# Kernel optimization log

Measured on AMD Instinct MI355X. Metric: run time of the kernel, lower is better.

## Reference

```python
import jax, jax.numpy as jnp
import numpy as np

N = 8192
F_IN = 256
F_OUT = 64
ALPHA = 0.2  # LeakyReLU negative slope
MASK_VAL = -9e15


def setup_inputs() -> dict:
    key = jax.random.key(0)
    k1, k2, k3, k4 = jax.random.split(key, 4)
    h = jax.random.normal(k1, (N, F_IN), dtype=jnp.float32)
    adj = jax.random.randint(k2, (N, N), 0, 2, dtype=jnp.int32)  # 0/1 dense adjacency
    # Parameters (original creates them inside forward with xavier init; here fixed inputs)
    W = jax.random.normal(k3, (F_IN, F_OUT), dtype=jnp.float32) * (1.414 * np.sqrt(2.0 / (F_IN + F_OUT)))
    a = jax.random.normal(k4, (2 * F_OUT, 1), dtype=jnp.float32) * (1.414 * np.sqrt(2.0 / (2 * F_OUT + 1)))
    return {"h": h, "adj": adj, "W": W, "a": a}


def reference(h, adj, W, a):
    # Wh: [N, F_OUT]
    Wh = h @ W
    # e_ij = LeakyReLU(a^T [Wh_i ; Wh_j]) computed via broadcast instead of the
    f_src = Wh @ a[:F_OUT, 0]   # [N] contribution of row node i
    f_dst = Wh @ a[F_OUT:, 0]   # [N] contribution of col node j
    e = jax.nn.leaky_relu(f_src[:, None] + f_dst[None, :], negative_slope=ALPHA)  # [N, N]
    # adj-masked row softmax
    scores = jnp.where(adj > 0, e, MASK_VAL)
    attention = jax.nn.softmax(scores, axis=1)
    # dropout omitted (deterministic eval reference)
    h_prime = attention @ Wh  # [N, F_OUT]
    return jax.nn.elu(h_prime)  # concat=True branch
```

## Files before the change

kernel.cpp:

```cpp
#include <hip/hip_runtime.h>
#include <hip/hip_bf16.h>

#define NN 8192
#define FIN 256
#define FOUT 64

typedef __attribute__((ext_vector_type(8))) short short8;
typedef __attribute__((ext_vector_type(4))) float f32x4;
typedef __attribute__((ext_vector_type(4))) int   iv4;

__device__ __forceinline__ unsigned short f2bf(float x){
  unsigned u = __float_as_uint(x);
  u += 0x7FFFu + ((u >> 16) & 1u);
  return (unsigned short)(u >> 16);
}

__global__ __launch_bounds__(256) void k_prep(const float* __restrict__ h,
    const float* __restrict__ W, const float* __restrict__ a,
    unsigned short* __restrict__ WhT, float* __restrict__ fs,
    float* __restrict__ fd, unsigned* __restrict__ gmax_u){
  __shared__ float Ws[128*64];
  __shared__ float hs[8][128];
  const int t = threadIdx.x, l = t & 63, wv = t >> 6;
  const int rb = blockIdx.x * 8;
  float acc0 = 0.f, acc1 = 0.f;
  for (int half = 0; half < 2; ++half){
    if (half) __syncthreads();
    for (int i = t; i < 2048; i += 256)
      ((float4*)Ws)[i] = ((const float4*)W)[half*2048 + i];
    {
      int rr = t >> 5, cc = t & 31;
      ((float4*)&hs[rr][0])[cc] =
          *(const float4*)(h + (size_t)(rb+rr)*FIN + half*128 + cc*4);
    }
    __syncthreads();
    #pragma unroll 8
    for (int k = 0; k < 128; ++k){
      float wval = Ws[k*64 + l];
      acc0 = fmaf(hs[wv*2+0][k], wval, acc0);
      acc1 = fmaf(hs[wv*2+1][k], wval, acc1);
    }
  }
  const int r0 = rb + wv*2, r1 = r0 + 1;
  float a1 = a[l], a2 = a[64 + l];
  float p0 = acc0*a1, q0 = acc0*a2, p1 = acc1*a1, q1 = acc1*a2;
  #pragma unroll
  for (int m = 1; m < 64; m <<= 1){
    p0 += __shfl_xor(p0, m); q0 += __shfl_xor(q0, m);
    p1 += __shfl_xor(p1, m); q1 += __shfl_xor(q1, m);
  }
  if (l == 0){
    fs[r0] = p0; fs[r1] = p1; fd[r0] = q0; fd[r1] = q1;
    atomicMax(gmax_u, __float_as_uint(q0 + 64.0f));
    atomicMax(gmax_u, __float_as_uint(q1 + 64.0f));
  }
  WhT[(size_t)l*NN + r0] = f2bf(acc0);
  WhT[(size_t)l*NN + r1] = f2bf(acc1);
}

struct Buf {
  iv4    a0, a1;
  float4 f0, f1;
  short8 w0, w1, w2, w3;
};

__device__ __forceinline__ void load_buf(Buf& b, const int* ap, const float* fp,
                                         const unsigned short* wp, int s){
  const int* aps = ap + s*32;
  b.a0 = __builtin_nontemporal_load((const iv4*)aps);
  b.a1 = __builtin_nontemporal_load(((const iv4*)aps) + 1);
  const float* fps = fp + s*32;
  b.f0 = *(const float4*)fps;
  b.f1 = *(const float4*)(fps + 4);
  const unsigned short* wps = wp + s*32;
  b.w0 = *(const short8*)(wps);
  b.w1 = *(const short8*)(wps + 16*NN);
  b.w2 = *(const short8*)(wps + 32*NN);
  b.w3 = *(const short8*)(wps + 48*NN);
}

__device__ __forceinline__ void step_buf(const Buf& b, float fsr, float mrow,
                                         f32x4* acc, float& sacc){
  const int   av[8] = {b.a0.x,b.a0.y,b.a0.z,b.a0.w, b.a1.x,b.a1.y,b.a1.z,b.a1.w};
  const float fv[8] = {b.f0.x,b.f0.y,b.f0.z,b.f0.w, b.f1.x,b.f1.y,b.f1.z,b.f1.w};
  float w[8];
  #pragma unroll
  for (int j = 0; j < 8; ++j){
    float x  = fsr + fv[j];
    float tt = fmaxf(x, 0.2f*x);
    float e  = __expf(tt - mrow);
    w[j] = (av[j] != 0) ? e : 0.0f;
    sacc += w[j];
  }
  short8 af;
  __hip_bfloat162* afp = (__hip_bfloat162*)&af;
  #pragma unroll
  for (int j = 0; j < 4; ++j)
    afp[j] = __float22bfloat162_rn(make_float2(w[2*j], w[2*j+1]));
  acc[0] = __builtin_amdgcn_mfma_f32_16x16x32_bf16(af, b.w0, acc[0], 0,0,0);
  acc[1] = __builtin_amdgcn_mfma_f32_16x16x32_bf16(af, b.w1, acc[1], 0,0,0);
  acc[2] = __builtin_amdgcn_mfma_f32_16x16x32_bf16(af, b.w2, acc[2], 0,0,0);
  acc[3] = __builtin_amdgcn_mfma_f32_16x16x32_bf16(af, b.w3, acc[3], 0,0,0);
}

__global__ __launch_bounds__(256, 2) void k_attn(const int* __restrict__ adj,
    const unsigned short* __restrict__ WhT, const float* __restrict__ fs,
    const float* __restrict__ fd, const unsigned* __restrict__ gmax_u,
    float* __restrict__ acc_out, float* __restrict__ s_out){
  const int l = threadIdx.x & 63;
  const int task = blockIdx.x*4 + (threadIdx.x >> 6);
  const int itile = task & 511, kchunk = task >> 9;
  const int ibase = itile*16, row = l & 15, quad = l >> 4;
  const float gmax = __uint_as_float(*gmax_u) - 64.0f;
  const float fsr  = fs[ibase + row];
  const float x0   = fsr + gmax;
  const float mrow = fmaxf(x0, 0.2f*x0);

  const size_t koff = (size_t)kchunk*2048 + quad*8;
  const int*            ap = adj + (size_t)(ibase+row)*NN + koff;
  const float*          fp = fd + koff;
  const unsigned short* wp = WhT + (size_t)row*NN + koff;

  f32x4 acc[4];
  #pragma unroll
  for (int nb = 0; nb < 4; ++nb) acc[nb] = (f32x4){0.f,0.f,0.f,0.f};

  Buf b0, b1, b2, b3;
  load_buf(b0, ap, fp, wp, 0);
  load_buf(b1, ap, fp, wp, 1);
  load_buf(b2, ap, fp, wp, 2);
  load_buf(b3, ap, fp, wp, 3);

  float sacc = 0.f;
  #pragma unroll 1
  for (int s = 0; s < 64; s += 4){
    step_buf(b0, fsr, mrow, acc, sacc); if (s+4 < 64) load_buf(b0, ap, fp, wp, s+4);
    step_buf(b1, fsr, mrow, acc, sacc); if (s+5 < 64) load_buf(b1, ap, fp, wp, s+5);
    step_buf(b2, fsr, mrow, acc, sacc); if (s+6 < 64) load_buf(b2, ap, fp, wp, s+6);
    step_buf(b3, fsr, mrow, acc, sacc); if (s+7 < 64) load_buf(b3, ap, fp, wp, s+7);
  }

  sacc += __shfl_xor(sacc, 16);
  sacc += __shfl_xor(sacc, 32);
  if (l < 16) s_out[kchunk*NN + ibase + l] = sacc;
  float* op = acc_out + ((size_t)kchunk*NN + ibase)*FOUT;
  #pragma unroll
  for (int nb = 0; nb < 4; ++nb)
    #pragma unroll
    for (int r = 0; r < 4; ++r)
      op[(quad*4 + r)*FOUT + nb*16 + row] = acc[nb][r];
}

__global__ __launch_bounds__(256) void k_out(const float* __restrict__ acc,
    const float* __restrict__ s, float* __restrict__ out){
  const int idx = blockIdx.x*256 + threadIdx.x;
  const int i = idx >> 6;
  float num = acc[idx] + acc[idx + NN*FOUT] + acc[idx + 2*NN*FOUT] + acc[idx + 3*NN*FOUT];
  float den = s[i] + s[i + NN] + s[i + 2*NN] + s[i + 3*NN];
  float x = num / den;
  out[idx] = (x > 0.f) ? x : (__expf(x) - 1.0f);
}

extern "C" void kernel_launch(void* const* d_in, const int* in_sizes, int n_in,
                              void* d_out, int out_size, void* d_ws, size_t ws_size,
                              hipStream_t stream){
  const float* h   = (const float*)d_in[0];
  const int*   adj = (const int*)d_in[1];
  const float* W   = (const float*)d_in[2];
  const float* a   = (const float*)d_in[3];
  char* ws = (char*)d_ws;
  unsigned short* WhT = (unsigned short*)ws;
  float*    fs     = (float*)(ws + (1u<<20));
  float*    fd     = (float*)(ws + (1u<<20) + 32768);
  unsigned* gmax_u = (unsigned*)(ws + (1u<<20) + 65536);
  float*    acc    = (float*)(ws + (2u<<20));
  float*    s_ws   = (float*)(ws + (2u<<20) + (size_t)4*NN*FOUT*4);

  (void)hipMemsetAsync(gmax_u, 0, 4, stream);
  k_prep<<<1024, 256, 0, stream>>>(h, W, a, WhT, fs, fd, gmax_u);
  k_attn<<<512, 256, 0, stream>>>(adj, WhT, fs, fd, gmax_u, acc, s_ws);
  k_out<<<2048, 256, 0, stream>>>(acc, s_ws, (float*)d_out);
}
```

Before: 526.5 us.

## Split prep GEMM into k-split stages and double attention k-chunks with decoupled prefetch

The Wh = h@W prep is rewritten as a k-split register-tiled GEMM writing partials, followed by a small reduction kernel that computes fs/fd, the global max and the transposed bf16 Wh. The attention kernel now splits K into 8 chunks instead of 4, launching twice the waves with occupancy hint 3. It prefetches adjacency four steps ahead but Wh/fd only two steps ahead to cut register use, and uses two partial sums. This adds an extra launch and more partial-sum traffic in the final combine kernel.

```diff
diff --git a/kernel.cpp b/kernel.cpp
--- a/kernel.cpp
+++ b/kernel.cpp
@@ -15,95 +15,107 @@
   return (unsigned short)(u >> 16);
 }
 
-__global__ __launch_bounds__(256) void k_prep(const float* __restrict__ h,
-    const float* __restrict__ W, const float* __restrict__ a,
-    unsigned short* __restrict__ WhT, float* __restrict__ fs,
-    float* __restrict__ fd, unsigned* __restrict__ gmax_u){
-  __shared__ float Ws[128*64];
-  __shared__ float hs[8][128];
+__global__ __launch_bounds__(256) void k_prep_a(const float* __restrict__ h,
+    const float* __restrict__ W, float* __restrict__ pWh){
+  __shared__ float hs[256][64];
+  const int t = threadIdx.x;
+  const int rowbase = (blockIdx.x & 31) * 256;
+  const int ks      = blockIdx.x >> 5;
+  const int kbase   = ks * 64;
+  #pragma unroll
+  for (int i = 0; i < 16; ++i){
+    int idx = i*256 + t;
+    int row = idx >> 4, kq = idx & 15;
+    float4 v = *(const float4*)(h + (size_t)(rowbase+row)*FIN + kbase + kq*4);
+    *(float4*)&hs[row][(kq ^ (row & 15)) * 4] = v;
+  }
+  __syncthreads();
+  const int l = t & 63, wv = t >> 6;
+  const int rr = wv*64 + l;
+  float acc[64];
+  #pragma unroll
+  for (int f = 0; f < 64; ++f) acc[f] = 0.f;
+  #pragma unroll 1
+  for (int kq = 0; kq < 16; ++kq){
+    float4 hv = *(const float4*)&hs[rr][(kq ^ (rr & 15)) * 4];
+    const float hj[4] = {hv.x, hv.y, hv.z, hv.w};
+    #pragma unroll
+    for (int j = 0; j < 4; ++j){
+      const float* wrow = W + (size_t)(kbase + kq*4 + j)*FOUT;
+      #pragma unroll
+      for (int f = 0; f < 64; ++f)
+        acc[f] = fmaf(hj[j], wrow[f], acc[f]);
+    }
+  }
+  float* op = pWh + (size_t)ks*(NN*FOUT) + (size_t)(rowbase + rr)*FOUT;
+  #pragma unroll
+  for (int f4 = 0; f4 < 16; ++f4)
+    *(float4*)(op + f4*4) = *(float4*)&acc[f4*4];
+}
+
+__global__ __launch_bounds__(256) void k_prep_b(const float* __restrict__ pWh,
+    const float* __restrict__ a, unsigned short* __restrict__ WhT,
+    float* __restrict__ fs, float* __restrict__ fd, unsigned* __restrict__ gmax_u){
   const int t = threadIdx.x, l = t & 63, wv = t >> 6;
-  const int rb = blockIdx.x * 8;
-  float acc0 = 0.f, acc1 = 0.f;
-  for (int half = 0; half < 2; ++half){
-    if (half) __syncthreads();
-    for (int i = t; i < 2048; i += 256)
-      ((float4*)Ws)[i] = ((const float4*)W)[half*2048 + i];
-    {
-      int rr = t >> 5, cc = t & 31;
-      ((float4*)&hs[rr][0])[cc] =
-          *(const float4*)(h + (size_t)(rb+rr)*FIN + half*128 + cc*4);
-    }
-    __syncthreads();
-    #pragma unroll 8
-    for (int k = 0; k < 128; ++k){
-      float wval = Ws[k*64 + l];
-      acc0 = fmaf(hs[wv*2+0][k], wval, acc0);
-      acc1 = fmaf(hs[wv*2+1][k], wval, acc1);
-    }
-  }
-  const int r0 = rb + wv*2, r1 = r0 + 1;
-  float a1 = a[l], a2 = a[64 + l];
-  float p0 = acc0*a1, q0 = acc0*a2, p1 = acc1*a1, q1 = acc1*a2;
+  const int row = blockIdx.x*4 + wv;
+  const size_t off = (size_t)row*FOUT + l;
+  float Wh = pWh[off] + pWh[off + NN*FOUT] + pWh[off + 2*NN*FOUT] + pWh[off + 3*NN*FOUT];
+  float p = Wh * a[l], q = Wh * a[64 + l];
   #pragma unroll
   for (int m = 1; m < 64; m <<= 1){
-    p0 += __shfl_xor(p0, m); q0 += __shfl_xor(q0, m);
-    p1 += __shfl_xor(p1, m); q1 += __shfl_xor(q1, m);
+    p += __shfl_xor(p, m); q += __shfl_xor(q, m);
   }
   if (l == 0){
-    fs[r0] = p0; fs[r1] = p1; fd[r0] = q0; fd[r1] = q1;
-    atomicMax(gmax_u, __float_as_uint(q0 + 64.0f));
-    atomicMax(gmax_u, __float_as_uint(q1 + 64.0f));
-  }
-  WhT[(size_t)l*NN + r0] = f2bf(acc0);
-  WhT[(size_t)l*NN + r1] = f2bf(acc1);
-}
-
-struct Buf {
-  iv4    a0, a1;
-  float4 f0, f1;
-  short8 w0, w1, w2, w3;
-};
-
-__device__ __forceinline__ void load_buf(Buf& b, const int* ap, const float* fp,
-                                         const unsigned short* wp, int s){
-  const int* aps = ap + s*32;
-  b.a0 = __builtin_nontemporal_load((const iv4*)aps);
-  b.a1 = __builtin_nontemporal_load(((const iv4*)aps) + 1);
-  const float* fps = fp + s*32;
-  b.f0 = *(const float4*)fps;
-  b.f1 = *(const float4*)(fps + 4);
+    fs[row] = p; fd[row] = q;
+    atomicMax(gmax_u, __float_as_uint(q + 64.0f));
+  }
+  WhT[(size_t)l*NN + row] = f2bf(Wh);
+}
+
+struct ABuf { iv4 a0, a1; };
+struct WBuf { float4 f0, f1; short8 w0, w1, w2, w3; };
+
+__device__ __forceinline__ void load_adj(ABuf& b, const int* ap, int s){
+  const iv4* p = (const iv4*)(ap + s*32);
+  b.a0 = __builtin_nontemporal_load(p);
+  b.a1 = __builtin_nontemporal_load(p + 1);
+}
+__device__ __forceinline__ void load_w(WBuf& b, const float* fp,
+                                       const unsigned short* wp, int s){
+  b.f0 = *(const float4*)(fp + s*32);
+  b.f1 = *(const float4*)(fp + s*32 + 4);
   const unsigned short* wps = wp + s*32;
   b.w0 = *(const short8*)(wps);
   b.w1 = *(const short8*)(wps + 16*NN);
   b.w2 = *(const short8*)(wps + 32*NN);
   b.w3 = *(const short8*)(wps + 48*NN);
 }
-
-__device__ __forceinline__ void step_buf(const Buf& b, float fsr, float mrow,
-                                         f32x4* acc, float& sacc){
-  const int   av[8] = {b.a0.x,b.a0.y,b.a0.z,b.a0.w, b.a1.x,b.a1.y,b.a1.z,b.a1.w};
-  const float fv[8] = {b.f0.x,b.f0.y,b.f0.z,b.f0.w, b.f1.x,b.f1.y,b.f1.z,b.f1.w};
+__device__ __forceinline__ void step(const ABuf& ab, const WBuf& wb,
+    float fsr, float mrow, f32x4* acc, float& s0, float& s1){
+  const int   av[8] = {ab.a0.x,ab.a0.y,ab.a0.z,ab.a0.w, ab.a1.x,ab.a1.y,ab.a1.z,ab.a1.w};
+  const float fv[8] = {wb.f0.x,wb.f0.y,wb.f0.z,wb.f0.w, wb.f1.x,wb.f1.y,wb.f1.z,wb.f1.w};
   float w[8];
   #pragma unroll
   for (int j = 0; j < 8; ++j){
-    float x  = fsr + fv[j];
+    float x = fsr + fv[j];
     float tt = fmaxf(x, 0.2f*x);
     float e  = __expf(tt - mrow);
     w[j] = (av[j] != 0) ? e : 0.0f;
-    sacc += w[j];
-  }
+  }
+  s0 += (w[0]+w[2]) + (w[4]+w[6]);
+  s1 += (w[1]+w[3]) + (w[5]+w[7]);
   short8 af;
   __hip_bfloat162* afp = (__hip_bfloat162*)&af;
   #pragma unroll
   for (int j = 0; j < 4; ++j)
     afp[j] = __float22bfloat162_rn(make_float2(w[2*j], w[2*j+1]));
-  acc[0] = __builtin_amdgcn_mfma_f32_16x16x32_bf16(af, b.w0, acc[0], 0,0,0);
-  acc[1] = __builtin_amdgcn_mfma_f32_16x16x32_bf16(af, b.w1, acc[1], 0,0,0);
-  acc[2] = __builtin_amdgcn_mfma_f32_16x16x32_bf16(af, b.w2, acc[2], 0,0,0);
-  acc[3] = __builtin_amdgcn_mfma_f32_16x16x32_bf16(af, b.w3, acc[3], 0,0,0);
-}
-
-__global__ __launch_bounds__(256, 2) void k_attn(const int* __restrict__ adj,
+  acc[0] = __builtin_amdgcn_mfma_f32_16x16x32_bf16(af, wb.w0, acc[0], 0,0,0);
+  acc[1] = __builtin_amdgcn_mfma_f32_16x16x32_bf16(af, wb.w1, acc[1], 0,0,0);
+  acc[2] = __builtin_amdgcn_mfma_f32_16x16x32_bf16(af, wb.w2, acc[2], 0,0,0);
+  acc[3] = __builtin_amdgcn_mfma_f32_16x16x32_bf16(af, wb.w3, acc[3], 0,0,0);
+}
+
+__global__ __launch_bounds__(256, 3) void k_attn(const int* __restrict__ adj,
     const unsigned short* __restrict__ WhT, const float* __restrict__ fs,
     const float* __restrict__ fd, const unsigned* __restrict__ gmax_u,
     float* __restrict__ acc_out, float* __restrict__ s_out){
@@ -116,7 +128,7 @@
   const float x0   = fsr + gmax;
   const float mrow = fmaxf(x0, 0.2f*x0);
 
-  const size_t koff = (size_t)kchunk*2048 + quad*8;
+  const size_t koff = (size_t)kchunk*1024 + quad*8;
   const int*            ap = adj + (size_t)(ibase+row)*NN + koff;
   const float*          fp = fd + koff;
   const unsigned short* wp = WhT + (size_t)row*NN + koff;
@@ -125,21 +137,25 @@
   #pragma unroll
   for (int nb = 0; nb < 4; ++nb) acc[nb] = (f32x4){0.f,0.f,0.f,0.f};
 
-  Buf b0, b1, b2, b3;
-  load_buf(b0, ap, fp, wp, 0);
-  load_buf(b1, ap, fp, wp, 1);
-  load_buf(b2, ap, fp, wp, 2);
-  load_buf(b3, ap, fp, wp, 3);
-
-  float sacc = 0.f;
+  ABuf ab0, ab1, ab2, ab3; WBuf wb0, wb1;
+  load_adj(ab0, ap, 0); load_adj(ab1, ap, 1);
+  load_adj(ab2, ap, 2); load_adj(ab3, ap, 3);
+  load_w(wb0, fp, wp, 0); load_w(wb1, fp, wp, 1);
+
+  float s0 = 0.f, s1 = 0.f;
   #pragma unroll 1
-  for (int s = 0; s < 64; s += 4){
-    step_buf(b0, fsr, mrow, acc, sacc); if (s+4 < 64) load_buf(b0, ap, fp, wp, s+4);
-    step_buf(b1, fsr, mrow, acc, sacc); if (s+5 < 64) load_buf(b1, ap, fp, wp, s+5);
-    step_buf(b2, fsr, mrow, acc, sacc); if (s+6 < 64) load_buf(b2, ap, fp, wp, s+6);
-    step_buf(b3, fsr, mrow, acc, sacc); if (s+7 < 64) load_buf(b3, ap, fp, wp, s+7);
-  }
-
+  for (int s = 0; s < 28; s += 4){
+    step(ab0, wb0, fsr, mrow, acc, s0, s1); load_adj(ab0, ap, s+4); load_w(wb0, fp, wp, s+2);
+    step(ab1, wb1, fsr, mrow, acc, s0, s1); load_adj(ab1, ap, s+5); load_w(wb1, fp, wp, s+3);
+    step(ab2, wb0, fsr, mrow, acc, s0, s1); load_adj(ab2, ap, s+6); load_w(wb0, fp, wp, s+4);
+    step(ab3, wb1, fsr, mrow, acc, s0, s1); load_adj(ab3, ap, s+7); load_w(wb1, fp, wp, s+5);
+  }
+  step(ab0, wb0, fsr, mrow, acc, s0, s1); load_w(wb0, fp, wp, 30);
+  step(ab1, wb1, fsr, mrow, acc, s0, s1); load_w(wb1, fp, wp, 31);
+  step(ab2, wb0, fsr, mrow, acc, s0, s1);
+  step(ab3, wb1, fsr, mrow, acc, s0, s1);
+
+  float sacc = s0 + s1;
   sacc += __shfl_xor(sacc, 16);
   sacc += __shfl_xor(sacc, 32);
   if (l < 16) s_out[kchunk*NN + ibase + l] = sacc;
@@ -155,8 +171,12 @@
     const float* __restrict__ s, float* __restrict__ out){
   const int idx = blockIdx.x*256 + threadIdx.x;
   const int i = idx >> 6;
-  float num = acc[idx] + acc[idx + NN*FOUT] + acc[idx + 2*NN*FOUT] + acc[idx + 3*NN*FOUT];
-  float den = s[i] + s[i + NN] + s[i + 2*NN] + s[i + 3*NN];
+  float num = 0.f, den = 0.f;
+  #pragma unroll
+  for (int ks = 0; ks < 8; ++ks){
+    num += acc[idx + (size_t)ks*(NN*FOUT)];
+    den += s[i + ks*NN];
+  }
   float x = num / den;
   out[idx] = (x > 0.f) ? x : (__expf(x) - 1.0f);
 }
@@ -173,11 +193,13 @@
   float*    fs     = (float*)(ws + (1u<<20));
   float*    fd     = (float*)(ws + (1u<<20) + 32768);
   unsigned* gmax_u = (unsigned*)(ws + (1u<<20) + 65536);
-  float*    acc    = (float*)(ws + (2u<<20));
-  float*    s_ws   = (float*)(ws + (2u<<20) + (size_t)4*NN*FOUT*4);
+  float*    pWh    = (float*)(ws + (2u<<20));
+  float*    acc    = (float*)(ws + (16u<<20));
+  float*    s_ws   = (float*)(ws + (32u<<20));
 
   (void)hipMemsetAsync(gmax_u, 0, 4, stream);
-  k_prep<<<1024, 256, 0, stream>>>(h, W, a, WhT, fs, fd, gmax_u);
-  k_attn<<<512, 256, 0, stream>>>(adj, WhT, fs, fd, gmax_u, acc, s_ws);
+  k_prep_a<<<128, 256, 0, stream>>>(h, W, pWh);
+  k_prep_b<<<2048, 256, 0, stream>>>(pWh, a, WhT, fs, fd, gmax_u);
+  k_attn<<<1024, 256, 0, stream>>>(adj, WhT, fs, fd, gmax_u, acc, s_ws);
   k_out<<<2048, 256, 0, stream>>>(acc, s_ws, (float*)d_out);
 }
```

New measurement: 552.2 us. 4.9% more time.
